# Performance work log

Measured on AMD Instinct MI355X. Metric: run time of the kernel, lower is better.

## Reference

```python
import jax, jax.numpy as jnp
import numpy as np
from jax import lax

N = 2048
P = 256
F_J = 0.05      # sparsity of recurrent matrix J
F_OUT = 0.05    # sparsity of readout
DT = 0.1
ON_TIME = 10
T = 200


def _activation(x):
    # Tanh_shifted_and_scaled: rates in [0, 1]
    return 0.5 * (1.0 + jnp.tanh(x))


def setup_inputs() -> dict:
    key = jax.random.key(0)
    k1, k2, k3, k4, k5 = jax.random.split(key, 5)
    # patterns ~ Uniform(-1, 1), shape [N, P]
    patterns = jax.random.uniform(k1, (N, P), jnp.float32, -1.0, 1.0)
    # sparse recurrent matrix J: gaussian values, density F_J, gain g
    g = 10.0 * 0.1 ** 0.25 / np.sqrt(N * P * np.sqrt(F_J))
    J_dense = jax.random.normal(k2, (N, N), jnp.float32) * jnp.float32(g)
    mask = jax.random.uniform(k3, (N, N)) < F_J
    J = jnp.where(mask, J_dense, 0.0).astype(jnp.float32)
    # sparse readout: ones at a random F_OUT fraction of units (frozen)
    w_out = (jax.random.uniform(k4, (N,)) < F_OUT).astype(jnp.float32)
    return {"patterns": patterns, "J": J, "w_out": w_out, "N_time_steps": T}


def reference(patterns, J, w_out, N_time_steps):
    # Batched over all P patterns at once (columns of [N, P] state).
    n = patterns.shape[0]
    x0 = jnp.zeros_like(patterns)           # [N, P]
    r0 = _activation(x0)

    def step(carry, ti):
        x, rates = carry
        inp = jnp.where(ti < ON_TIME, patterns, 0.0)      # [N, P]
        x = x + DT * (-x + J @ rates + inp)               # [N, P]
        rates = _activation(x)
        out_t = w_out @ rates                             # [P]
        return (x, rates), out_t

    _, outs = lax.scan(step, (x0, r0), jnp.arange(N_time_steps))  # [T, P]
    readout = outs.T / n                                   # [P, T]
    return readout
```

## Files before the change

### kernel.cpp

```cpp
#include <hip/hip_runtime.h>
#include <hip/hip_bf16.h>


#define NN 2048
#define PP 256
#define DT_C 0.1f
#define ON_TIME_C 10

typedef __attribute__((ext_vector_type(8)))  short bf16x8;
typedef __attribute__((ext_vector_type(16))) float f32x16;

__device__ __forceinline__ unsigned short bf16rne(float f) {
    unsigned b = __float_as_uint(f);
    return (unsigned short)((b + 0x7FFFu + ((b >> 16) & 1u)) >> 16);
}
__device__ __forceinline__ int kperm16(int s) {
    return (s & 3) + (((s >> 2) & 1) << 3) + ((s >> 3) << 2);
}

__global__ void convert_J_kernel(const float* __restrict__ J,
                                 unsigned short* __restrict__ Jp) {
    int i = blockIdx.x * blockDim.x + threadIdx.x;
    int row = i >> 11, k = i & 2047;
    Jp[((size_t)row << 11) + (k & ~15) + kperm16(k & 15)] = bf16rne(J[i]);
}

__global__ void init_kernel(float* __restrict__ x,
                            unsigned short* __restrict__ rT,
                            float* __restrict__ out, int nout) {
    int i = blockIdx.x * blockDim.x + threadIdx.x;
    x[i] = 0.0f;
    rT[i] = 0x3F00;
    if (i < nout) out[i] = 0.0f;
}

#define AS1 __attribute__((address_space(1)))
#define AS3 __attribute__((address_space(3)))
#define GLOAD16(g, l) \
    __builtin_amdgcn_global_load_lds((const AS1 void*)(g), (AS3 void*)(l), 16, 0, 0)

__global__ __launch_bounds__(512, 1) void gemm_step_kernel(
    const unsigned short* __restrict__ Jp,
    const unsigned short* __restrict__ rin,
    unsigned short* __restrict__ rout,
    float* __restrict__ x, const float* __restrict__ patterns,
    const float* __restrict__ w_out, float* __restrict__ out,
    int t, int T, int with_input) {

    __shared__ char smem[98304];

    const int tid  = threadIdx.x;
    const int w    = tid >> 6;
    const int lane = tid & 63;
    const int s    = w >> 2;
    const int kq   = w & 3;
    const int h    = lane >> 5;

    const int bid   = (blockIdx.x & 7) * 32 + (blockIdx.x >> 3);
    const int mbase = (bid >> 3) * 64;
    const int nbase = (bid & 7) * 32;

    const int rA0 = 8 * w + (lane >> 4);
    const int rA1 = rA0 + 4;
    const int rB  = 4 * w + (lane >> 4);
    const char* gA0 = (const char*)Jp  + (((size_t)(mbase + rA0)) << 12)
                      + (((lane & 15) ^ (rA0 & 15)) << 4);
    const char* gA1 = (const char*)Jp  + (((size_t)(mbase + rA1)) << 12)
                      + (((lane & 15) ^ (rA1 & 15)) << 4);
    const char* gB  = (const char*)rin + (((size_t)(nbase + rB )) << 12)
                      + (((lane & 15) ^ (rB  & 15)) << 4);
    const int ldsA0 = (8 * w) * 256, ldsA1 = (8 * w + 4) * 256;
    const int ldsB  = 16384 + 4 * w * 256;

    const int rA = 32 * s + (lane & 31);
    const int rBn = lane & 31;

    f32x16 acc = {};

    GLOAD16(gA0,       smem + 0 * 24576 + ldsA0);
    GLOAD16(gA1,       smem + 0 * 24576 + ldsA1);
    GLOAD16(gB,        smem + 0 * 24576 + ldsB);
    GLOAD16(gA0 + 256, smem + 1 * 24576 + ldsA0);
    GLOAD16(gA1 + 256, smem + 1 * 24576 + ldsA1);
    GLOAD16(gB  + 256, smem + 1 * 24576 + ldsB);

    #pragma unroll
    for (int ph = 0; ph < 16; ++ph) {
        if (ph < 14) {
            const int bo = ((ph + 2) & 3) * 24576;
            GLOAD16(gA0 + (ph + 2) * 256, smem + bo + ldsA0);
            GLOAD16(gA1 + (ph + 2) * 256, smem + bo + ldsA1);
            GLOAD16(gB  + (ph + 2) * 256, smem + bo + ldsB);
        }
        if (ph < 14)       asm volatile("s_waitcnt vmcnt(6)" ::: "memory");
        else if (ph == 14) asm volatile("s_waitcnt vmcnt(3)" ::: "memory");
        else               asm volatile("s_waitcnt vmcnt(0)" ::: "memory");
        __builtin_amdgcn_s_barrier();
        __builtin_amdgcn_sched_barrier(0);

        const int bb = (ph & 3) * 24576;
        #pragma unroll
        for (int sl = 0; sl < 2; ++sl) {
            const int c = kq * 4 + sl * 2 + h;
            bf16x8 a = *(const bf16x8*)(smem + bb + rA * 256
                                        + ((c ^ (rA & 15)) << 4));
            bf16x8 b = *(const bf16x8*)(smem + bb + 16384 + rBn * 256
                                        + ((c ^ (rBn & 15)) << 4));
            acc = __builtin_amdgcn_mfma_f32_32x32x16_bf16(a, b, acc, 0, 0, 0);
        }
    }

    __syncthreads();

    {
        float* pf = (float*)smem;
        const int plane = (s * 4 + kq) * 1024;
        #pragma unroll
        for (int reg = 0; reg < 16; ++reg) {
            int row = (reg & 3) + 8 * (reg >> 2) + 4 * h;
            pf[plane + row * 32 + (lane & 31)] = acc[reg];
        }
    }
    __syncthreads();

    {
        const int s2 = tid >> 8, rr = (tid >> 3) & 31, c4 = (tid & 7) * 4;
        const float4* pf4 = (const float4*)smem;
        int base = ((s2 * 4) * 1024 + rr * 32 + c4) >> 2;
        float4 v0 = pf4[base], v1 = pf4[base + 256];
        float4 v2 = pf4[base + 512], v3 = pf4[base + 768];
        float sum[4] = {v0.x + v1.x + v2.x + v3.x, v0.y + v1.y + v2.y + v3.y,
                        v0.z + v1.z + v2.z + v3.z, v0.w + v1.w + v2.w + v3.w};

        const int mloc = s2 * 32 + rr;
        const int m = mbase + mloc;
        const int n0 = nbase + c4;
        size_t xo = ((size_t)m << 8) + n0;
        float4 xv = *(const float4*)(x + xo);
        float4 pv = make_float4(0.f, 0.f, 0.f, 0.f);
        if (with_input) pv = *(const float4*)(patterns + xo);
        float wsc = (w_out[m] != 0.0f) ? (1.0f / (float)NN) : 0.0f;

        float xn[4] = {xv.x + DT_C * (sum[0] + pv.x - xv.x),
                       xv.y + DT_C * (sum[1] + pv.y - xv.y),
                       xv.z + DT_C * (sum[2] + pv.z - xv.z),
                       xv.w + DT_C * (sum[3] + pv.w - xv.w)};
        *(float4*)(x + xo) = make_float4(xn[0], xn[1], xn[2], xn[3]);

        const int pos = (mloc & ~15) + kperm16(mloc & 15);
        #pragma unroll
        for (int j = 0; j < 4; ++j) {
            float r = 0.5f * (1.0f + tanhf(xn[j]));
            if (wsc != 0.0f)
                atomicAdd(&out[(size_t)(n0 + j) * T + t], r * wsc);
            int nloc = c4 + j;
            int byte = 32768 + nloc * 128
                     + (((pos >> 3) ^ (nloc & 7)) << 4) + (pos & 7) * 2;
            *(unsigned short*)(smem + byte) = bf16rne(r);
        }
    }
    __syncthreads();
    if (tid < 256) {
        int nl = tid >> 3, p = tid & 7;
        uint4 v = *(const uint4*)(smem + 32768 + nl * 128 + ((p ^ (nl & 7)) << 4));
        *(uint4*)((char*)rout + (((size_t)(nbase + nl)) << 12) + mbase * 2 + p * 16) = v;
    }
}

extern "C" void kernel_launch(void* const* d_in, const int* in_sizes, int n_in,
                              void* d_out, int out_size, void* d_ws, size_t ws_size,
                              hipStream_t stream) {
    const float* patterns = (const float*)d_in[0];
    const float* J        = (const float*)d_in[1];
    const float* w_out    = (const float*)d_in[2];
    float* out            = (float*)d_out;

    int T = out_size / PP;

    size_t off = 0;
    auto alloc = [&](size_t bytes) {
        void* p = (char*)d_ws + off;
        off += (bytes + 255) & ~(size_t)255;
        return p;
    };
    unsigned short* Jp = (unsigned short*)alloc((size_t)NN * NN * 2);
    unsigned short* r0 = (unsigned short*)alloc((size_t)PP * NN * 2);
    unsigned short* r1 = (unsigned short*)alloc((size_t)PP * NN * 2);
    float*          x  = (float*)         alloc((size_t)NN * PP * 4);
    (void)ws_size; (void)n_in; (void)in_sizes;

    convert_J_kernel<<<(NN * NN) / 256, 256, 0, stream>>>(J, Jp);
    init_kernel<<<(NN * PP) / 256, 256, 0, stream>>>(x, r0, out, PP * T);

    for (int t = 0; t < T; ++t) {
        const unsigned short* rin = (t & 1) ? r1 : r0;
        unsigned short*      rout = (t & 1) ? r0 : r1;
        gemm_step_kernel<<<256, 512, 0, stream>>>(Jp, rin, rout, x, patterns,
                                                  w_out, out, t, T,
                                                  (t < ON_TIME_C) ? 1 : 0);
    }
}
```

Before: 1.932 ms.

## Double block to 1024 threads with 8-way K split and double-buffered loads

```diff
diff --git a/kernel.cpp b/kernel.cpp
--- a/kernel.cpp
+++ b/kernel.cpp
@@ -39,7 +39,7 @@
 #define GLOAD16(g, l) \
     __builtin_amdgcn_global_load_lds((const AS1 void*)(g), (AS3 void*)(l), 16, 0, 0)
 
-__global__ __launch_bounds__(512, 1) void gemm_step_kernel(
+__global__ __launch_bounds__(1024, 1) void gemm_step_kernel(
     const unsigned short* __restrict__ Jp,
     const unsigned short* __restrict__ rin,
     unsigned short* __restrict__ rout,
@@ -50,61 +50,57 @@
     __shared__ char smem[98304];
 
     const int tid  = threadIdx.x;
-    const int w    = tid >> 6;
+    const int wv   = tid >> 6;
     const int lane = tid & 63;
-    const int s    = w >> 2;
-    const int kq   = w & 3;
+    const int s    = wv >> 3;
+    const int kq   = wv & 7;
     const int h    = lane >> 5;
 
     const int bid   = (blockIdx.x & 7) * 32 + (blockIdx.x >> 3);
     const int mbase = (bid >> 3) * 64;
     const int nbase = (bid & 7) * 32;
 
-    const int rA0 = 8 * w + (lane >> 4);
-    const int rA1 = rA0 + 4;
-    const int rB  = 4 * w + (lane >> 4);
-    const char* gA0 = (const char*)Jp  + (((size_t)(mbase + rA0)) << 12)
-                      + (((lane & 15) ^ (rA0 & 15)) << 4);
-    const char* gA1 = (const char*)Jp  + (((size_t)(mbase + rA1)) << 12)
-                      + (((lane & 15) ^ (rA1 & 15)) << 4);
-    const char* gB  = (const char*)rin + (((size_t)(nbase + rB )) << 12)
-                      + (((lane & 15) ^ (rB  & 15)) << 4);
-    const int ldsA0 = (8 * w) * 256, ldsA1 = (8 * w + 4) * 256;
-    const int ldsB  = 16384 + 4 * w * 256;
+    const int p   = tid & 31;
+    const int ra0 = tid >> 5;
+    const int ra1 = 32 + ra0;
+    const char* gA0 = (const char*)Jp  + (((size_t)(mbase + ra0)) << 12)
+                      + ((p ^ (ra0 & 15)) << 4);
+    const char* gA1 = (const char*)Jp  + (((size_t)(mbase + ra1)) << 12)
+                      + ((p ^ (ra1 & 15)) << 4);
+    const char* gB  = (const char*)rin + (((size_t)(nbase + ra0)) << 12)
+                      + ((p ^ (ra0 & 15)) << 4);
+    const int ldsA0 = 1024 * wv;
+    const int ldsA1 = 16384 + 1024 * wv;
+    const int ldsB  = 32768 + 1024 * wv;
 
-    const int rA = 32 * s + (lane & 31);
+    const int rA  = 32 * s + (lane & 31);
     const int rBn = lane & 31;
 
     f32x16 acc = {};
 
-    GLOAD16(gA0,       smem + 0 * 24576 + ldsA0);
-    GLOAD16(gA1,       smem + 0 * 24576 + ldsA1);
-    GLOAD16(gB,        smem + 0 * 24576 + ldsB);
-    GLOAD16(gA0 + 256, smem + 1 * 24576 + ldsA0);
-    GLOAD16(gA1 + 256, smem + 1 * 24576 + ldsA1);
-    GLOAD16(gB  + 256, smem + 1 * 24576 + ldsB);
+    GLOAD16(gA0, smem + ldsA0);
+    GLOAD16(gA1, smem + ldsA1);
+    GLOAD16(gB,  smem + ldsB);
 
     #pragma unroll
-    for (int ph = 0; ph < 16; ++ph) {
-        if (ph < 14) {
-            const int bo = ((ph + 2) & 3) * 24576;
-            GLOAD16(gA0 + (ph + 2) * 256, smem + bo + ldsA0);
-            GLOAD16(gA1 + (ph + 2) * 256, smem + bo + ldsA1);
-            GLOAD16(gB  + (ph + 2) * 256, smem + bo + ldsB);
+    for (int ph = 0; ph < 8; ++ph) {
+        asm volatile("s_waitcnt vmcnt(0)" ::: "memory");
+        __builtin_amdgcn_s_barrier();
+        if (ph < 7) {
+            const int bo = ((ph + 1) & 1) * 49152;
+            GLOAD16(gA0 + (ph + 1) * 512, smem + bo + ldsA0);
+            GLOAD16(gA1 + (ph + 1) * 512, smem + bo + ldsA1);
+            GLOAD16(gB  + (ph + 1) * 512, smem + bo + ldsB);
         }
-        if (ph < 14)       asm volatile("s_waitcnt vmcnt(6)" ::: "memory");
-        else if (ph == 14) asm volatile("s_waitcnt vmcnt(3)" ::: "memory");
-        else               asm volatile("s_waitcnt vmcnt(0)" ::: "memory");
-        __builtin_amdgcn_s_barrier();
         __builtin_amdgcn_sched_barrier(0);
 
-        const int bb = (ph & 3) * 24576;
+        const int bb = (ph & 1) * 49152;
         #pragma unroll
         for (int sl = 0; sl < 2; ++sl) {
-            const int c = kq * 4 + sl * 2 + h;
-            bf16x8 a = *(const bf16x8*)(smem + bb + rA * 256
+            const int c = (kq * 2 + sl) * 2 + h;
+            bf16x8 a = *(const bf16x8*)(smem + bb + rA * 512
                                         + ((c ^ (rA & 15)) << 4));
-            bf16x8 b = *(const bf16x8*)(smem + bb + 16384 + rBn * 256
+            bf16x8 b = *(const bf16x8*)(smem + bb + 32768 + rBn * 512
                                         + ((c ^ (rBn & 15)) << 4));
             acc = __builtin_amdgcn_mfma_f32_32x32x16_bf16(a, b, acc, 0, 0, 0);
         }
@@ -114,7 +110,7 @@
 
     {
         float* pf = (float*)smem;
-        const int plane = (s * 4 + kq) * 1024;
+        const int plane = (s * 8 + kq) * 1024;
         #pragma unroll
         for (int reg = 0; reg < 16; ++reg) {
             int row = (reg & 3) + 8 * (reg >> 2) + 4 * h;
@@ -124,46 +120,46 @@
     __syncthreads();
 
     {
-        const int s2 = tid >> 8, rr = (tid >> 3) & 31, c4 = (tid & 7) * 4;
-        const float4* pf4 = (const float4*)smem;
-        int base = ((s2 * 4) * 1024 + rr * 32 + c4) >> 2;
-        float4 v0 = pf4[base], v1 = pf4[base + 256];
-        float4 v2 = pf4[base + 512], v3 = pf4[base + 768];
-        float sum[4] = {v0.x + v1.x + v2.x + v3.x, v0.y + v1.y + v2.y + v3.y,
-                        v0.z + v1.z + v2.z + v3.z, v0.w + v1.w + v2.w + v3.w};
+        const int mloc = tid >> 4;
+        const int c2   = (tid & 15) * 2;
+        const int s2   = mloc >> 5;
+        const float* pf = (const float*)smem;
+        float2 sum = make_float2(0.f, 0.f);
+        #pragma unroll
+        for (int q = 0; q < 8; ++q) {
+            float2 v = *(const float2*)(pf + (s2 * 8 + q) * 1024
+                                        + (mloc & 31) * 32 + c2);
+            sum.x += v.x; sum.y += v.y;
+        }
 
-        const int mloc = s2 * 32 + rr;
-        const int m = mbase + mloc;
-        const int n0 = nbase + c4;
+        const int m  = mbase + mloc;
+        const int n0 = nbase + c2;
         size_t xo = ((size_t)m << 8) + n0;
-        float4 xv = *(const float4*)(x + xo);
-        float4 pv = make_float4(0.f, 0.f, 0.f, 0.f);
-        if (with_input) pv = *(const float4*)(patterns + xo);
+        float2 xv = *(const float2*)(x + xo);
+        float2 pv = make_float2(0.f, 0.f);
+        if (with_input) pv = *(const float2*)(patterns + xo);
         float wsc = (w_out[m] != 0.0f) ? (1.0f / (float)NN) : 0.0f;
 
-        float xn[4] = {xv.x + DT_C * (sum[0] + pv.x - xv.x),
-                       xv.y + DT_C * (sum[1] + pv.y - xv.y),
-                       xv.z + DT_C * (sum[2] + pv.z - xv.z),
-                       xv.w + DT_C * (sum[3] + pv.w - xv.w)};
-        *(float4*)(x + xo) = make_float4(xn[0], xn[1], xn[2], xn[3]);
-
+        float xn0 = xv.x + DT_C * (sum.x + pv.x - xv.x);
+        float xn1 = xv.y + DT_C * (sum.y + pv.y - xv.y);
+        *(float2*)(x + xo) = make_float2(xn0, xn1);
+        float r0f = 0.5f * (1.0f + tanhf(xn0));
+        float r1f = 0.5f * (1.0f + tanhf(xn1));
+        if (wsc != 0.0f) {
+            atomicAdd(&out[(size_t)n0 * T + t],       r0f * wsc);
+            atomicAdd(&out[(size_t)(n0 + 1) * T + t], r1f * wsc);
+        }
         const int pos = (mloc & ~15) + kperm16(mloc & 15);
-        #pragma unroll
-        for (int j = 0; j < 4; ++j) {
-            float r = 0.5f * (1.0f + tanhf(xn[j]));
-            if (wsc != 0.0f)
-                atomicAdd(&out[(size_t)(n0 + j) * T + t], r * wsc);
-            int nloc = c4 + j;
-            int byte = 32768 + nloc * 128
-                     + (((pos >> 3) ^ (nloc & 7)) << 4) + (pos & 7) * 2;
-            *(unsigned short*)(smem + byte) = bf16rne(r);
-        }
+        int b0 = 65536 + c2 * 128       + (((pos >> 3) ^ (c2 & 7)) << 4)       + (pos & 7) * 2;
+        int b1 = 65536 + (c2 + 1) * 128 + (((pos >> 3) ^ ((c2 + 1) & 7)) << 4) + (pos & 7) * 2;
+        *(unsigned short*)(smem + b0) = bf16rne(r0f);
+        *(unsigned short*)(smem + b1) = bf16rne(r1f);
     }
     __syncthreads();
     if (tid < 256) {
-        int nl = tid >> 3, p = tid & 7;
-        uint4 v = *(const uint4*)(smem + 32768 + nl * 128 + ((p ^ (nl & 7)) << 4));
-        *(uint4*)((char*)rout + (((size_t)(nbase + nl)) << 12) + mbase * 2 + p * 16) = v;
+        int nl = tid >> 3, pc = tid & 7;
+        uint4 v = *(const uint4*)(smem + 65536 + nl * 128 + ((pc ^ (nl & 7)) << 4));
+        *(uint4*)((char*)rout + (((size_t)(nbase + nl)) << 12) + mbase * 2 + pc * 16) = v;
     }
 }
 
@@ -195,8 +191,8 @@
     for (int t = 0; t < T; ++t) {
         const unsigned short* rin = (t & 1) ? r1 : r0;
         unsigned short*      rout = (t & 1) ? r0 : r1;
-        gemm_step_kernel<<<256, 512, 0, stream>>>(Jp, rin, rout, x, patterns,
-                                                  w_out, out, t, T,
-                                                  (t < ON_TIME_C) ? 1 : 0);
+        gemm_step_kernel<<<256, 1024, 0, stream>>>(Jp, rin, rout, x, patterns,
+                                                   w_out, out, t, T,
+                                                   (t < ON_TIME_C) ? 1 : 0);
     }
 }
```

After: 2.265 ms. +17.3%, slower.

## Deepen LDS prefetch ring to six stages and hoist epilogue loads

Applied to the files above, without the earlier changes.

```diff
diff --git a/kernel.cpp b/kernel.cpp
--- a/kernel.cpp
+++ b/kernel.cpp
@@ -47,7 +47,7 @@
     const float* __restrict__ w_out, float* __restrict__ out,
     int t, int T, int with_input) {
 
-    __shared__ char smem[98304];
+    __shared__ char smem[147456];
 
     const int tid  = threadIdx.x;
     const int w    = tid >> 6;
@@ -72,33 +72,45 @@
     const int ldsA0 = (8 * w) * 256, ldsA1 = (8 * w + 4) * 256;
     const int ldsB  = 16384 + 4 * w * 256;
 
-    const int rA = 32 * s + (lane & 31);
+    const int rA  = 32 * s + (lane & 31);
     const int rBn = lane & 31;
 
+    const int e_s2 = tid >> 8, e_rr = (tid >> 3) & 31, e_c4 = (tid & 7) * 4;
+    const int e_mloc = e_s2 * 32 + e_rr;
+    const int e_m  = mbase + e_mloc;
+    const int e_n0 = nbase + e_c4;
+    const size_t e_xo = ((size_t)e_m << 8) + e_n0;
+    float4 e_xv = *(const float4*)(x + e_xo);
+    float4 e_pv = make_float4(0.f, 0.f, 0.f, 0.f);
+    if (with_input) e_pv = *(const float4*)(patterns + e_xo);
+    float e_wsc = (w_out[e_m] != 0.0f) ? (1.0f / (float)NN) : 0.0f;
+
     f32x16 acc = {};
 
-    GLOAD16(gA0,       smem + 0 * 24576 + ldsA0);
-    GLOAD16(gA1,       smem + 0 * 24576 + ldsA1);
-    GLOAD16(gB,        smem + 0 * 24576 + ldsB);
-    GLOAD16(gA0 + 256, smem + 1 * 24576 + ldsA0);
-    GLOAD16(gA1 + 256, smem + 1 * 24576 + ldsA1);
-    GLOAD16(gB  + 256, smem + 1 * 24576 + ldsB);
+    #pragma unroll
+    for (int ps = 0; ps < 4; ++ps) {
+        GLOAD16(gA0 + ps * 256, smem + ps * 24576 + ldsA0);
+        GLOAD16(gA1 + ps * 256, smem + ps * 24576 + ldsA1);
+        GLOAD16(gB  + ps * 256, smem + ps * 24576 + ldsB);
+    }
 
     #pragma unroll
     for (int ph = 0; ph < 16; ++ph) {
-        if (ph < 14) {
-            const int bo = ((ph + 2) & 3) * 24576;
-            GLOAD16(gA0 + (ph + 2) * 256, smem + bo + ldsA0);
-            GLOAD16(gA1 + (ph + 2) * 256, smem + bo + ldsA1);
-            GLOAD16(gB  + (ph + 2) * 256, smem + bo + ldsB);
-        }
-        if (ph < 14)       asm volatile("s_waitcnt vmcnt(6)" ::: "memory");
-        else if (ph == 14) asm volatile("s_waitcnt vmcnt(3)" ::: "memory");
-        else               asm volatile("s_waitcnt vmcnt(0)" ::: "memory");
+        if (ph < 12) {
+            const int bo = ((ph + 4) % 6) * 24576;
+            GLOAD16(gA0 + (ph + 4) * 256, smem + bo + ldsA0);
+            GLOAD16(gA1 + (ph + 4) * 256, smem + bo + ldsA1);
+            GLOAD16(gB  + (ph + 4) * 256, smem + bo + ldsB);
+        }
+        if (ph < 12)       asm volatile("s_waitcnt vmcnt(12)" ::: "memory");
+        else if (ph == 12) asm volatile("s_waitcnt vmcnt(9)"  ::: "memory");
+        else if (ph == 13) asm volatile("s_waitcnt vmcnt(6)"  ::: "memory");
+        else if (ph == 14) asm volatile("s_waitcnt vmcnt(3)"  ::: "memory");
+        else               asm volatile("s_waitcnt vmcnt(0)"  ::: "memory");
         __builtin_amdgcn_s_barrier();
         __builtin_amdgcn_sched_barrier(0);
 
-        const int bb = (ph & 3) * 24576;
+        const int bb = (ph % 6) * 24576;
         #pragma unroll
         for (int sl = 0; sl < 2; ++sl) {
             const int c = kq * 4 + sl * 2 + h;
@@ -124,36 +136,26 @@
     __syncthreads();
 
     {
-        const int s2 = tid >> 8, rr = (tid >> 3) & 31, c4 = (tid & 7) * 4;
         const float4* pf4 = (const float4*)smem;
-        int base = ((s2 * 4) * 1024 + rr * 32 + c4) >> 2;
+        int base = ((e_s2 * 4) * 1024 + e_rr * 32 + e_c4) >> 2;
         float4 v0 = pf4[base], v1 = pf4[base + 256];
         float4 v2 = pf4[base + 512], v3 = pf4[base + 768];
         float sum[4] = {v0.x + v1.x + v2.x + v3.x, v0.y + v1.y + v2.y + v3.y,
                         v0.z + v1.z + v2.z + v3.z, v0.w + v1.w + v2.w + v3.w};
 
-        const int mloc = s2 * 32 + rr;
-        const int m = mbase + mloc;
-        const int n0 = nbase + c4;
-        size_t xo = ((size_t)m << 8) + n0;
-        float4 xv = *(const float4*)(x + xo);
-        float4 pv = make_float4(0.f, 0.f, 0.f, 0.f);
-        if (with_input) pv = *(const float4*)(patterns + xo);
-        float wsc = (w_out[m] != 0.0f) ? (1.0f / (float)NN) : 0.0f;
-
-        float xn[4] = {xv.x + DT_C * (sum[0] + pv.x - xv.x),
-                       xv.y + DT_C * (sum[1] + pv.y - xv.y),
-                       xv.z + DT_C * (sum[2] + pv.z - xv.z),
-                       xv.w + DT_C * (sum[3] + pv.w - xv.w)};
-        *(float4*)(x + xo) = make_float4(xn[0], xn[1], xn[2], xn[3]);
-
-        const int pos = (mloc & ~15) + kperm16(mloc & 15);
+        float xn[4] = {e_xv.x + DT_C * (sum[0] + e_pv.x - e_xv.x),
+                       e_xv.y + DT_C * (sum[1] + e_pv.y - e_xv.y),
+                       e_xv.z + DT_C * (sum[2] + e_pv.z - e_xv.z),
+                       e_xv.w + DT_C * (sum[3] + e_pv.w - e_xv.w)};
+        *(float4*)(x + e_xo) = make_float4(xn[0], xn[1], xn[2], xn[3]);
+
+        const int pos = (e_mloc & ~15) + kperm16(e_mloc & 15);
         #pragma unroll
         for (int j = 0; j < 4; ++j) {
             float r = 0.5f * (1.0f + tanhf(xn[j]));
-            if (wsc != 0.0f)
-                atomicAdd(&out[(size_t)(n0 + j) * T + t], r * wsc);
-            int nloc = c4 + j;
+            if (e_wsc != 0.0f)
+                atomicAdd(&out[(size_t)(e_n0 + j) * T + t], r * e_wsc);
+            int nloc = e_c4 + j;
             int byte = 32768 + nloc * 128
                      + (((pos >> 3) ^ (nloc & 7)) << 4) + (pos & 7) * 2;
             *(unsigned short*)(smem + byte) = bf16rne(r);
@@ -161,9 +163,9 @@
     }
     __syncthreads();
     if (tid < 256) {
-        int nl = tid >> 3, p = tid & 7;
-        uint4 v = *(const uint4*)(smem + 32768 + nl * 128 + ((p ^ (nl & 7)) << 4));
-        *(uint4*)((char*)rout + (((size_t)(nbase + nl)) << 12) + mbase * 2 + p * 16) = v;
+        int nl = tid >> 3, pc = tid & 7;
+        uint4 v = *(const uint4*)(smem + 32768 + nl * 128 + ((pc ^ (nl & 7)) << 4));
+        *(uint4*)((char*)rout + (((size_t)(nbase + nl)) << 12) + mbase * 2 + pc * 16) = v;
     }
 }
 
```

Result: no change. 1.942 ms (+0.5%).
